# Performance work log

Hardware: AMD Instinct MI355X
Metric: run time of the kernel (lower is better)

## Reference

```python
import jax, jax.numpy as jnp
import numpy as np

V, E, H, D, A = 10000, 256, 256, 256, 256  # vocab, emb, enc_hid, dec_hid, attn_dim
B, S = 128, 64


def setup_inputs() -> dict:
    key = jax.random.key(0)
    ks = jax.random.split(key, 20)
    rn = lambda k, shp, sc: jax.random.normal(k, shp, jnp.float32) * sc
    tokens = jax.random.randint(ks[0], (B, S), 0, V, dtype=jnp.int32)
    inp = jnp.stack([tokens, jnp.ones_like(tokens)], axis=-1)  # [B,S,2], ch1 = mask
    s = 0.05
    return {
        "input": inp,
        "emb_table": rn(ks[1], (V, E), s),
        "enc_Wih_f": rn(ks[2], (3 * H, E), s), "enc_Whh_f": rn(ks[3], (3 * H, H), s),
        "enc_bih_f": rn(ks[4], (3 * H,), s), "enc_bhh_f": rn(ks[5], (3 * H,), s),
        "enc_Wih_b": rn(ks[6], (3 * H, E), s), "enc_Whh_b": rn(ks[7], (3 * H, H), s),
        "enc_bih_b": rn(ks[8], (3 * H,), s), "enc_bhh_b": rn(ks[9], (3 * H,), s),
        "enc_fc_W": rn(ks[10], (D, 2 * H), s), "enc_fc_b": rn(ks[11], (D,), s),
        "attn_W": rn(ks[12], (A, 2 * H + D), s), "attn_b": rn(ks[13], (A,), s),
        "dec_Wih": rn(ks[14], (3 * D, 2 * H + E), s), "dec_Whh": rn(ks[15], (3 * D, D), s),
        "dec_bih": rn(ks[16], (3 * D,), s), "dec_bhh": rn(ks[17], (3 * D,), s),
        "out_W": rn(ks[18], (V, 2 * H + D + E), s), "out_b": rn(ks[19], (V,), s),
    }


def _gru_cell(xp, h, Whh, bhh):
    # xp = x @ Wih.T + bih already computed; PyTorch gate order r,z,n
    rx, zx, nx = jnp.split(xp, 3, axis=-1)
    rh, zh, nh = jnp.split(h @ Whh.T + bhh, 3, axis=-1)
    r = jax.nn.sigmoid(rx + rh)
    z = jax.nn.sigmoid(zx + zh)
    n = jnp.tanh(nx + r * nh)
    return (1.0 - z) * n + z * h


def _gru_dir(x, Wih, Whh, bih, bhh, reverse):
    # x: [B,S,E] -> outputs [B,S,Hd], final hidden [B,Hd]
    xp = jnp.einsum('bse,ge->bsg', x, Wih) + bih  # [B,S,3Hd]
    Hd = Whh.shape[1]

    def step(h, xpt):
        h = _gru_cell(xpt, h, Whh, bhh)
        return h, h

    h0 = jnp.zeros((x.shape[0], Hd), x.dtype)
    hT, ys = jax.lax.scan(step, h0, jnp.swapaxes(xp, 0, 1), reverse=reverse)
    return jnp.swapaxes(ys, 0, 1), hT


def reference(input, emb_table, enc_Wih_f, enc_Whh_f, enc_bih_f, enc_bhh_f,
              enc_Wih_b, enc_Whh_b, enc_bih_b, enc_bhh_b, enc_fc_W, enc_fc_b,
              attn_W, attn_b, dec_Wih, dec_Whh, dec_bih, dec_bhh, out_W, out_b):
    b, s = input.shape[0], input.shape[1]
    v = emb_table.shape[0]
    tok = input[:, :, 0]
    mask = input[:, :, 1].astype(jnp.float32)
    emb = emb_table[tok] * mask[:, :, None]  # [B,S,E]

    # bidirectional encoder
    f_out, f_h = _gru_dir(emb, enc_Wih_f, enc_Whh_f, enc_bih_f, enc_bhh_f, False)
    b_out, b_h = _gru_dir(emb, enc_Wih_b, enc_Whh_b, enc_bih_b, enc_bhh_b, True)
    enc_out = jnp.concatenate([f_out, b_out], axis=-1)  # [B,S,2H]
    hidden = jnp.tanh(jnp.concatenate([f_h, b_h], axis=-1) @ enc_fc_W.T + enc_fc_b)  # [B,D]

    d = hidden.shape[1]

    def dec_step(carry, _):
        tok_t, h = carry
        e = emb_table[tok_t]  # [B,E]
        rep = jnp.concatenate(
            [jnp.broadcast_to(h[:, None, :], (b, s, d)), enc_out], axis=-1)
        energy = jnp.tanh(jnp.einsum('bsf,af->bsa', rep, attn_W) + attn_b)
        a = jax.nn.softmax(jnp.sum(energy, axis=-1), axis=1)  # [B,S]
        w = jnp.einsum('bs,bsh->bh', a, enc_out)  # [B,2H]
        rnn_in = jnp.concatenate([e, w], axis=-1)
        xp = rnn_in @ dec_Wih.T + dec_bih
        h_new = _gru_cell(xp, h, dec_Whh, dec_bhh)
        logits = jnp.concatenate([h_new, w, e], axis=-1) @ out_W.T + out_b  # [B,V]
        tok_new = jnp.argmax(logits, axis=-1).astype(tok_t.dtype)
        return (tok_new, h_new), logits

    tok0 = jnp.zeros((b,), jnp.int32)
    (_, _), outs = jax.lax.scan(dec_step, (tok0, hidden), None, length=s - 1)
    first = jnp.zeros((b, v), jnp.float32).at[:, 0].set(1.0)  # outputs[:,0] one-hot
    outputs = jnp.concatenate([first[:, None, :], jnp.swapaxes(outs, 0, 1)], axis=1)
    return jax.nn.log_softmax(outputs.reshape(-1, v), axis=-1)
```

## Files before the change

### kernel.cpp

```cpp
#include <hip/hip_runtime.h>
#include <math.h>


__device__ __forceinline__ float dot4(const float4 a, const float4 b) {
    return fmaf(a.x, b.x, fmaf(a.y, b.y, fmaf(a.z, b.z, a.w * b.w)));
}

__global__ void embed_kernel(const int* __restrict__ inp, const float* __restrict__ table,
                             float* __restrict__ emb) {
    int bs = blockIdx.x;
    int tok = inp[bs * 2];
    float msk = (float)inp[bs * 2 + 1];
    emb[bs * 256 + threadIdx.x] = table[tok * 256 + threadIdx.x] * msk;
}

__global__ __launch_bounds__(256) void enc_step_kernel(
    const float* __restrict__ emb,
    const float* __restrict__ Wih_f, const float* __restrict__ Whh_f,
    const float* __restrict__ bih_f, const float* __restrict__ bhh_f,
    const float* __restrict__ Wih_b, const float* __restrict__ Whh_b,
    const float* __restrict__ bih_b, const float* __restrict__ bhh_b,
    const float* __restrict__ hin_f, float* __restrict__ hout_f,
    const float* __restrict__ hin_b, float* __restrict__ hout_b,
    float* __restrict__ enc_out, int step)
{
    const int dir = blockIdx.y;
    const float* Wih = dir ? Wih_b : Wih_f;
    const float* Whh = dir ? Whh_b : Whh_f;
    const float* bih = dir ? bih_b : bih_f;
    const float* bhh = dir ? bhh_b : bhh_f;
    const float* hin = dir ? hin_b : hin_f;
    float* hout = dir ? hout_b : hout_f;
    const int t = dir ? (63 - step) : step;

    const int tid = threadIdx.x;
    const int dl = tid & 31;
    const int bsub = tid >> 5;
    const int d0 = (blockIdx.x & 7) * 32;
    const int b0 = (blockIdx.x >> 3) * 8;
    const int d = d0 + dl;
    const int b = b0 + bsub;

    __shared__ float xs[8][256];
    __shared__ float hs[8][256];
    for (int i = tid; i < 2048; i += 256) {
        int bl = i >> 8, e = i & 255;
        int bb = b0 + bl;
        xs[bl][e] = emb[(bb * 64 + t) * 256 + e];
        hs[bl][e] = hin[bb * 256 + e];
    }
    __syncthreads();

    const float4* x4 = (const float4*)xs[bsub];
    const float4* h4 = (const float4*)hs[bsub];
    const float4* wr_i = (const float4*)(Wih + (size_t)d * 256);
    const float4* wz_i = (const float4*)(Wih + (size_t)(256 + d) * 256);
    const float4* wn_i = (const float4*)(Wih + (size_t)(512 + d) * 256);
    const float4* wr_h = (const float4*)(Whh + (size_t)d * 256);
    const float4* wz_h = (const float4*)(Whh + (size_t)(256 + d) * 256);
    const float4* wn_h = (const float4*)(Whh + (size_t)(512 + d) * 256);

    float rs = 0.f, zs = 0.f, nx = 0.f, nh = 0.f;
    for (int k = 0; k < 64; ++k) {
        float4 xv = x4[k];
        float4 hv = h4[k];
        rs += dot4(xv, wr_i[k]) + dot4(hv, wr_h[k]);
        zs += dot4(xv, wz_i[k]) + dot4(hv, wz_h[k]);
        nx += dot4(xv, wn_i[k]);
        nh += dot4(hv, wn_h[k]);
    }
    rs += bih[d] + bhh[d];
    zs += bih[256 + d] + bhh[256 + d];
    nx += bih[512 + d];
    nh += bhh[512 + d];

    float r = 1.0f / (1.0f + expf(-rs));
    float z = 1.0f / (1.0f + expf(-zs));
    float n = tanhf(nx + r * nh);
    float hprev = hs[bsub][d];
    float hn = (1.0f - z) * n + z * hprev;

    hout[b * 256 + d] = hn;
    enc_out[(b * 64 + t) * 512 + dir * 256 + d] = hn;
}

__global__ __launch_bounds__(256) void enc_fc_kernel(
    const float* __restrict__ hf, const float* __restrict__ hb,
    const float* __restrict__ W, const float* __restrict__ bias,
    float* __restrict__ hdec0)
{
    int b = blockIdx.x, tid = threadIdx.x;
    __shared__ float xs[512];
    xs[tid] = hf[b * 256 + tid];
    xs[256 + tid] = hb[b * 256 + tid];
    __syncthreads();
    const float4* w4 = (const float4*)(W + (size_t)tid * 512);
    const float4* x4 = (const float4*)xs;
    float s = 0.f;
    for (int k = 0; k < 128; ++k) s += dot4(x4[k], w4[k]);
    hdec0[b * 256 + tid] = tanhf(s + bias[tid]);
}

#define GP 68
__global__ __launch_bounds__(256) void gemm2_kernel(
    const float* __restrict__ Amat, int lda,
    const float* __restrict__ Wmat, int ldw,
    const float* __restrict__ bias,
    float* __restrict__ C, long ldc,
    int N, int K)
{
    const int tid = threadIdx.x;
    const int tn = tid & 15;
    const int tm = tid >> 4;
    const long m0 = (long)blockIdx.y * 64;
    const int n0 = blockIdx.x * 64;
    __shared__ float As[64][GP];
    __shared__ float Ws[64][GP];

    const float* Abase = Amat + (m0 + tm) * lda + tn * 4;
    float4 ar[4], wr[4];
    float acc[4][4] = {};

    {
#pragma unroll
        for (int q = 0; q < 4; ++q)
            ar[q] = *(const float4*)(Abase + (long)16 * q * lda);
#pragma unroll
        for (int q = 0; q < 4; ++q) {
            int n = n0 + tm + 16 * q;
            wr[q] = (n < N) ? *(const float4*)(Wmat + (long)n * ldw + tn * 4)
                            : make_float4(0.f, 0.f, 0.f, 0.f);
        }
    }

    int k0 = 0;
    while (true) {
#pragma unroll
        for (int q = 0; q < 4; ++q) {
            *(float4*)&As[tm + 16 * q][tn * 4] = ar[q];
            *(float4*)&Ws[tm + 16 * q][tn * 4] = wr[q];
        }
        __syncthreads();

        const int kn = k0 + 64;
        if (kn < K) {
#pragma unroll
            for (int q = 0; q < 4; ++q)
                ar[q] = *(const float4*)(Abase + (long)16 * q * lda + kn);
#pragma unroll
            for (int q = 0; q < 4; ++q) {
                int n = n0 + tm + 16 * q;
                wr[q] = (n < N) ? *(const float4*)(Wmat + (long)n * ldw + tn * 4 + kn)
                                : make_float4(0.f, 0.f, 0.f, 0.f);
            }
        }

#pragma unroll
        for (int kk = 0; kk < 64; kk += 4) {
            float4 av[4], wv[4];
#pragma unroll
            for (int i = 0; i < 4; ++i) av[i] = *(const float4*)&As[tm + 16 * i][kk];
#pragma unroll
            for (int j = 0; j < 4; ++j) wv[j] = *(const float4*)&Ws[tn + 16 * j][kk];
#pragma unroll
            for (int i = 0; i < 4; ++i)
#pragma unroll
                for (int j = 0; j < 4; ++j)
                    acc[i][j] += dot4(av[i], wv[j]);
        }

        if (kn >= K) break;
        __syncthreads();
        k0 = kn;
    }

#pragma unroll
    for (int i = 0; i < 4; ++i) {
        long m = m0 + tm + 16 * i;
#pragma unroll
        for (int j = 0; j < 4; ++j) {
            int n = n0 + tn + 16 * j;
            if (n < N) C[m * ldc + n] = acc[i][j] + bias[n];
        }
    }
}

__global__ __launch_bounds__(256) void attn_kernel(
    const float* __restrict__ hprev, const float* __restrict__ attn_W,
    const float* __restrict__ enc_att, const float* __restrict__ enc_out,
    float* __restrict__ feat)
{
    const int b = blockIdx.x, tid = threadIdx.x;
    __shared__ float hsh[256];
    __shared__ float hE[256];
    __shared__ float part[256];
    __shared__ float aw[64];

    hsh[tid] = hprev[b * 256 + tid];
    __syncthreads();
    {
        const float4* w4 = (const float4*)(attn_W + (size_t)tid * 768);
        const float4* h4 = (const float4*)hsh;
        float s = 0.f;
        for (int k = 0; k < 64; ++k) s += dot4(h4[k], w4[k]);
        hE[tid] = s;
    }
    __syncthreads();
    {
        const int si = tid & 63, g = tid >> 6;
        const float* ea = enc_att + ((size_t)b * 64 + si) * 256 + g * 64;
        const float* he = hE + g * 64;
        float p = 0.f;
        for (int a = 0; a < 64; ++a) p += tanhf(he[a] + ea[a]);
        part[tid] = p;
    }
    __syncthreads();
    if (tid < 64) {
        float sc = part[tid] + part[64 + tid] + part[128 + tid] + part[192 + tid];
        float m = sc;
        for (int off = 32; off; off >>= 1) m = fmaxf(m, __shfl_xor(m, off));
        float ex = expf(sc - m);
        float sum = ex;
        for (int off = 32; off; off >>= 1) sum += __shfl_xor(sum, off);
        aw[tid] = ex / sum;
    }
    __syncthreads();
    {
        float w0 = 0.f, w1 = 0.f;
        for (int s2 = 0; s2 < 64; ++s2) {
            float as = aw[s2];
            const float* eo = enc_out + ((size_t)b * 64 + s2) * 512;
            w0 = fmaf(as, eo[tid], w0);
            w1 = fmaf(as, eo[256 + tid], w1);
        }
        feat[b * 1024 + 256 + tid] = w0;
        feat[b * 1024 + 512 + tid] = w1;
    }
}

__global__ __launch_bounds__(256) void dec_gru_kernel(
    const float* __restrict__ feat, const float* __restrict__ hin,
    const float* __restrict__ Wih, const float* __restrict__ Whh,
    const float* __restrict__ bih, const float* __restrict__ bhh,
    float* __restrict__ hout, float* __restrict__ feat_h)
{
    const int tid = threadIdx.x;
    const int dl = tid & 31, bsub = tid >> 5;
    const int d0 = (blockIdx.x & 7) * 32, b0 = (blockIdx.x >> 3) * 8;
    const int d = d0 + dl, b = b0 + bsub;

    __shared__ float rin[8][768];
    __shared__ float hsh[8][256];
    for (int i = tid; i < 2048; i += 256) {
        int bl = i >> 8, k = i & 255;
        rin[bl][k] = feat[(b0 + bl) * 1024 + 768 + k];
    }
    for (int i = tid; i < 4096; i += 256) {
        int bl = i >> 9, k = i & 511;
        rin[bl][256 + k] = feat[(b0 + bl) * 1024 + 256 + k];
    }
    for (int i = tid; i < 2048; i += 256) {
        int bl = i >> 8, k = i & 255;
        hsh[bl][k] = hin[(b0 + bl) * 256 + k];
    }
    __syncthreads();

    const float4* xv4 = (const float4*)rin[bsub];
    const float4* hv4 = (const float4*)hsh[bsub];
    const float4* Wr = (const float4*)(Wih + (size_t)d * 768);
    const float4* Wz = (const float4*)(Wih + (size_t)(256 + d) * 768);
    const float4* Wn = (const float4*)(Wih + (size_t)(512 + d) * 768);
    const float4* Ur = (const float4*)(Whh + (size_t)d * 256);
    const float4* Uz = (const float4*)(Whh + (size_t)(256 + d) * 256);
    const float4* Un = (const float4*)(Whh + (size_t)(512 + d) * 256);

    float rs = 0.f, zs = 0.f, nx = 0.f, nh = 0.f;
    for (int k = 0; k < 192; ++k) {
        float4 xv = xv4[k];
        rs += dot4(xv, Wr[k]);
        zs += dot4(xv, Wz[k]);
        nx += dot4(xv, Wn[k]);
    }
    for (int k = 0; k < 64; ++k) {
        float4 hv = hv4[k];
        rs += dot4(hv, Ur[k]);
        zs += dot4(hv, Uz[k]);
        nh += dot4(hv, Un[k]);
    }
    rs += bih[d] + bhh[d];
    zs += bih[256 + d] + bhh[256 + d];
    nx += bih[512 + d];
    nh += bhh[512 + d];

    float r = 1.0f / (1.0f + expf(-rs));
    float z = 1.0f / (1.0f + expf(-zs));
    float n = tanhf(nx + r * nh);
    float hprev = hsh[bsub][d];
    float hn = (1.0f - z) * n + z * hprev;

    hout[b * 256 + d] = hn;
    feat_h[b * 1024 + d] = hn;
}

__global__ __launch_bounds__(256) void argmax_kernel(
    const float* __restrict__ logits, const float* __restrict__ table,
    int* __restrict__ tok, float* __restrict__ feat)
{
    const int b = blockIdx.x, tid = threadIdx.x;
    const float4* row4 = (const float4*)(logits + (long)b * 640000);
    float best = -3.402823466e38f;
    int bi = 0;
    for (int v4 = tid; v4 < 2500; v4 += 256) {
        float4 x = row4[v4];
        int base = v4 << 2;
        if (x.x > best) { best = x.x; bi = base; }
        if (x.y > best) { best = x.y; bi = base + 1; }
        if (x.z > best) { best = x.z; bi = base + 2; }
        if (x.w > best) { best = x.w; bi = base + 3; }
    }
    __shared__ float bv[256];
    __shared__ int bix[256];
    bv[tid] = best; bix[tid] = bi;
    __syncthreads();
    for (int s2 = 128; s2; s2 >>= 1) {
        if (tid < s2) {
            float o = bv[tid + s2]; int oi = bix[tid + s2];
            if (o > bv[tid] || (o == bv[tid] && oi < bix[tid])) { bv[tid] = o; bix[tid] = oi; }
        }
        __syncthreads();
    }
    int t0 = bix[0];
    if (tid == 0) tok[b] = t0;
    feat[b * 1024 + 768 + tid] = table[(size_t)t0 * 256 + tid];
}

__global__ void init_e_kernel(const float* __restrict__ table, float* __restrict__ feat) {
    feat[blockIdx.x * 1024 + 768 + threadIdx.x] = table[threadIdx.x];
}

__global__ __launch_bounds__(256) void logsoftmax_kernel(float* __restrict__ out) {
    const int row = blockIdx.x;
    float* p = out + (long)row * 10000;
    const int tid = threadIdx.x;
    __shared__ float red[256];

    if ((row & 63) == 0) {
        float lse = logf(expf(1.0f) + 9999.0f);
        for (int v = tid; v < 10000; v += 256) p[v] = (v == 0 ? 1.0f : 0.0f) - lse;
        return;
    }

    float vals[40];
    float m = -3.402823466e38f;
#pragma unroll
    for (int i = 0; i < 40; ++i) {
        int v = tid + (i << 8);
        vals[i] = (v < 10000) ? p[v] : -3.402823466e38f;
        m = fmaxf(m, vals[i]);
    }
    red[tid] = m; __syncthreads();
    for (int s2 = 128; s2; s2 >>= 1) { if (tid < s2) red[tid] = fmaxf(red[tid], red[tid + s2]); __syncthreads(); }
    m = red[0]; __syncthreads();

    float sum = 0.f;
#pragma unroll
    for (int i = 0; i < 40; ++i) {
        int v = tid + (i << 8);
        if (v < 10000) sum += expf(vals[i] - m);
    }
    red[tid] = sum; __syncthreads();
    for (int s2 = 128; s2; s2 >>= 1) { if (tid < s2) red[tid] += red[tid + s2]; __syncthreads(); }
    float lse = m + logf(red[0]);

#pragma unroll
    for (int i = 0; i < 40; ++i) {
        int v = tid + (i << 8);
        if (v < 10000) p[v] = vals[i] - lse;
    }
}

extern "C" void kernel_launch(void* const* d_in, const int* in_sizes, int n_in,
                              void* d_out, int out_size, void* d_ws, size_t ws_size,
                              hipStream_t stream)
{
    const int*   inp      = (const int*)d_in[0];
    const float* emb_tab  = (const float*)d_in[1];
    const float* eWih_f   = (const float*)d_in[2];
    const float* eWhh_f   = (const float*)d_in[3];
    const float* ebih_f   = (const float*)d_in[4];
    const float* ebhh_f   = (const float*)d_in[5];
    const float* eWih_b   = (const float*)d_in[6];
    const float* eWhh_b   = (const float*)d_in[7];
    const float* ebih_b   = (const float*)d_in[8];
    const float* ebhh_b   = (const float*)d_in[9];
    const float* fc_W     = (const float*)d_in[10];
    const float* fc_b     = (const float*)d_in[11];
    const float* attn_W   = (const float*)d_in[12];
    const float* attn_b   = (const float*)d_in[13];
    const float* dWih     = (const float*)d_in[14];
    const float* dWhh     = (const float*)d_in[15];
    const float* dbih     = (const float*)d_in[16];
    const float* dbhh     = (const float*)d_in[17];
    const float* out_W    = (const float*)d_in[18];
    const float* out_b    = (const float*)d_in[19];

    float* ws = (float*)d_ws;
    float* emb     = ws;
    float* enc_out = emb + 2097152;
    float* enc_att = enc_out + 4194304;
    float* hf      = enc_att + 2097152;
    float* hb      = hf + 65536;
    float* hdec    = hb + 65536;
    float* feat    = hdec + 65536;
    int*   tok     = (int*)(feat + 131072);
    float* out     = (float*)d_out;

    embed_kernel<<<8192, 256, 0, stream>>>(inp, emb_tab, emb);
    hipMemsetAsync(hf, 0, 32768 * sizeof(float), stream);
    hipMemsetAsync(hb, 0, 32768 * sizeof(float), stream);
    for (int i = 0; i < 64; ++i) {
        const float* hinf = hf + (i & 1) * 32768;
        float* houtf = hf + ((i + 1) & 1) * 32768;
        const float* hinb = hb + (i & 1) * 32768;
        float* houtb = hb + ((i + 1) & 1) * 32768;
        enc_step_kernel<<<dim3(128, 2), 256, 0, stream>>>(
            emb, eWih_f, eWhh_f, ebih_f, ebhh_f, eWih_b, eWhh_b, ebih_b, ebhh_b,
            hinf, houtf, hinb, houtb, enc_out, i);
    }
    enc_fc_kernel<<<128, 256, 0, stream>>>(hf, hb, fc_W, fc_b, hdec);

    gemm2_kernel<<<dim3(4, 128), 256, 0, stream>>>(
        enc_out, 512, attn_W + 256, 768, attn_b, enc_att, 256, 256, 512);

    init_e_kernel<<<128, 256, 0, stream>>>(emb_tab, feat);

    for (int t = 1; t < 64; ++t) {
        const float* hprev = hdec + ((t - 1) & 1) * 32768;
        float* hcur = hdec + (t & 1) * 32768;
        attn_kernel<<<128, 256, 0, stream>>>(hprev, attn_W, enc_att, enc_out, feat);
        dec_gru_kernel<<<128, 256, 0, stream>>>(feat, hprev, dWih, dWhh, dbih, dbhh, hcur, feat);
        gemm2_kernel<<<dim3(157, 2), 256, 0, stream>>>(
            feat, 1024, out_W, 1024, out_b, out + (long)t * 10000, 640000, 10000, 1024);
        if (t < 63)
            argmax_kernel<<<128, 256, 0, stream>>>(out + (long)t * 10000, emb_tab, tok, feat);
    }

    logsoftmax_kernel<<<8192, 256, 0, stream>>>(out);
}
```

Baseline: 20.00 ms.

## Replace per-step encoder and decoder launches with persistent cooperative grid-sync kernels

The 64 encoder step launches and the roughly 250 decoder launches (attention, GRU, output GEMM, argmax) are replaced by two persistent cooperative kernels that loop over time steps and use grid.sync between phases. In the decoder, argmax for step t and attention for step t+1 run on disjoint block ranges in the same phase, and the output GEMM tiles are spread over all resident blocks. The aim is to remove kernel launch overhead and idle gaps between the many small dependent kernels. In exchange each step pays for grid-wide barriers, and the cooperative launch can fail if the grid does not fit, in which case the code falls back to the old launch loops.

```diff
diff --git a/kernel.cpp b/kernel.cpp
--- a/kernel.cpp
+++ b/kernel.cpp
@@ -1,5 +1,8 @@
 #include <hip/hip_runtime.h>
+#include <hip/hip_cooperative_groups.h>
 #include <math.h>
+
+namespace cg = cooperative_groups;
 
 
 __device__ __forceinline__ float dot4(const float4 a, const float4 b) {
@@ -12,6 +15,65 @@
     int tok = inp[bs * 2];
     float msk = (float)inp[bs * 2 + 1];
     emb[bs * 256 + threadIdx.x] = table[tok * 256 + threadIdx.x] * msk;
+}
+
+__device__ __forceinline__ void enc_step_phase(
+    int dir, int bx, int step,
+    const float* __restrict__ emb,
+    const float* __restrict__ Wih, const float* __restrict__ Whh,
+    const float* __restrict__ bih, const float* __restrict__ bhh,
+    const float* __restrict__ hin, float* __restrict__ hout,
+    float* __restrict__ enc_out,
+    float (*xs)[256], float (*hs)[256])
+{
+    const int t = dir ? (63 - step) : step;
+    const int tid = threadIdx.x;
+    const int dl = tid & 31;
+    const int bsub = tid >> 5;
+    const int d0 = (bx & 7) * 32;
+    const int b0 = (bx >> 3) * 8;
+    const int d = d0 + dl;
+    const int b = b0 + bsub;
+
+    for (int i = tid; i < 2048; i += 256) {
+        int bl = i >> 8, e = i & 255;
+        int bb = b0 + bl;
+        xs[bl][e] = emb[(bb * 64 + t) * 256 + e];
+        hs[bl][e] = hin[bb * 256 + e];
+    }
+    __syncthreads();
+
+    const float4* x4 = (const float4*)xs[bsub];
+    const float4* h4 = (const float4*)hs[bsub];
+    const float4* wr_i = (const float4*)(Wih + (size_t)d * 256);
+    const float4* wz_i = (const float4*)(Wih + (size_t)(256 + d) * 256);
+    const float4* wn_i = (const float4*)(Wih + (size_t)(512 + d) * 256);
+    const float4* wr_h = (const float4*)(Whh + (size_t)d * 256);
+    const float4* wz_h = (const float4*)(Whh + (size_t)(256 + d) * 256);
+    const float4* wn_h = (const float4*)(Whh + (size_t)(512 + d) * 256);
+
+    float rs = 0.f, zs = 0.f, nx = 0.f, nh = 0.f;
+    for (int k = 0; k < 64; ++k) {
+        float4 xv = x4[k];
+        float4 hv = h4[k];
+        rs += dot4(xv, wr_i[k]) + dot4(hv, wr_h[k]);
+        zs += dot4(xv, wz_i[k]) + dot4(hv, wz_h[k]);
+        nx += dot4(xv, wn_i[k]);
+        nh += dot4(hv, wn_h[k]);
+    }
+    rs += bih[d] + bhh[d];
+    zs += bih[256 + d] + bhh[256 + d];
+    nx += bih[512 + d];
+    nh += bhh[512 + d];
+
+    float r = 1.0f / (1.0f + expf(-rs));
+    float z = 1.0f / (1.0f + expf(-zs));
+    float n = tanhf(nx + r * nh);
+    float hprev = hs[bsub][d];
+    float hn = (1.0f - z) * n + z * hprev;
+
+    hout[b * 256 + d] = hn;
+    enc_out[(b * 64 + t) * 512 + dir * 256 + d] = hn;
 }
 
 __global__ __launch_bounds__(256) void enc_step_kernel(
@@ -25,63 +87,42 @@
     float* __restrict__ enc_out, int step)
 {
     const int dir = blockIdx.y;
+    __shared__ __align__(16) float xs[8][256];
+    __shared__ __align__(16) float hs[8][256];
+    enc_step_phase(dir, blockIdx.x, step, emb,
+                   dir ? Wih_b : Wih_f, dir ? Whh_b : Whh_f,
+                   dir ? bih_b : bih_f, dir ? bhh_b : bhh_f,
+                   dir ? hin_b : hin_f, dir ? hout_b : hout_f,
+                   enc_out, xs, hs);
+}
+
+__global__ __launch_bounds__(256) void enc_loop_kernel(
+    const float* __restrict__ emb,
+    const float* __restrict__ Wih_f, const float* __restrict__ Whh_f,
+    const float* __restrict__ bih_f, const float* __restrict__ bhh_f,
+    const float* __restrict__ Wih_b, const float* __restrict__ Whh_b,
+    const float* __restrict__ bih_b, const float* __restrict__ bhh_b,
+    float* __restrict__ hf, float* __restrict__ hb,
+    float* __restrict__ enc_out)
+{
+    cg::grid_group grid = cg::this_grid();
+    const int dir = blockIdx.x & 1;
+    const int bx = blockIdx.x >> 1;
     const float* Wih = dir ? Wih_b : Wih_f;
     const float* Whh = dir ? Whh_b : Whh_f;
     const float* bih = dir ? bih_b : bih_f;
     const float* bhh = dir ? bhh_b : bhh_f;
-    const float* hin = dir ? hin_b : hin_f;
-    float* hout = dir ? hout_b : hout_f;
-    const int t = dir ? (63 - step) : step;
-
-    const int tid = threadIdx.x;
-    const int dl = tid & 31;
-    const int bsub = tid >> 5;
-    const int d0 = (blockIdx.x & 7) * 32;
-    const int b0 = (blockIdx.x >> 3) * 8;
-    const int d = d0 + dl;
-    const int b = b0 + bsub;
-
-    __shared__ float xs[8][256];
-    __shared__ float hs[8][256];
-    for (int i = tid; i < 2048; i += 256) {
-        int bl = i >> 8, e = i & 255;
-        int bb = b0 + bl;
-        xs[bl][e] = emb[(bb * 64 + t) * 256 + e];
-        hs[bl][e] = hin[bb * 256 + e];
-    }
-    __syncthreads();
-
-    const float4* x4 = (const float4*)xs[bsub];
-    const float4* h4 = (const float4*)hs[bsub];
-    const float4* wr_i = (const float4*)(Wih + (size_t)d * 256);
-    const float4* wz_i = (const float4*)(Wih + (size_t)(256 + d) * 256);
-    const float4* wn_i = (const float4*)(Wih + (size_t)(512 + d) * 256);
-    const float4* wr_h = (const float4*)(Whh + (size_t)d * 256);
-    const float4* wz_h = (const float4*)(Whh + (size_t)(256 + d) * 256);
-    const float4* wn_h = (const float4*)(Whh + (size_t)(512 + d) * 256);
-
-    float rs = 0.f, zs = 0.f, nx = 0.f, nh = 0.f;
-    for (int k = 0; k < 64; ++k) {
-        float4 xv = x4[k];
-        float4 hv = h4[k];
-        rs += dot4(xv, wr_i[k]) + dot4(hv, wr_h[k]);
-        zs += dot4(xv, wz_i[k]) + dot4(hv, wz_h[k]);
-        nx += dot4(xv, wn_i[k]);
-        nh += dot4(hv, wn_h[k]);
-    }
-    rs += bih[d] + bhh[d];
-    zs += bih[256 + d] + bhh[256 + d];
-    nx += bih[512 + d];
-    nh += bhh[512 + d];
-
-    float r = 1.0f / (1.0f + expf(-rs));
-    float z = 1.0f / (1.0f + expf(-zs));
-    float n = tanhf(nx + r * nh);
-    float hprev = hs[bsub][d];
-    float hn = (1.0f - z) * n + z * hprev;
-
-    hout[b * 256 + d] = hn;
-    enc_out[(b * 64 + t) * 512 + dir * 256 + d] = hn;
+    float* hbase = dir ? hb : hf;
+
+    __shared__ __align__(16) float xs[8][256];
+    __shared__ __align__(16) float hs[8][256];
+
+    for (int i = 0; i < 64; ++i) {
+        const float* hin = hbase + (i & 1) * 32768;
+        float* hout = hbase + ((i + 1) & 1) * 32768;
+        enc_step_phase(dir, bx, i, emb, Wih, Whh, bih, bhh, hin, hout, enc_out, xs, hs);
+        if (i != 63) grid.sync();
+    }
 }
 
 __global__ __launch_bounds__(256) void enc_fc_kernel(
@@ -90,7 +131,7 @@
     float* __restrict__ hdec0)
 {
     int b = blockIdx.x, tid = threadIdx.x;
-    __shared__ float xs[512];
+    __shared__ __align__(16) float xs[512];
     xs[tid] = hf[b * 256 + tid];
     xs[256 + tid] = hb[b * 256 + tid];
     __syncthreads();
@@ -102,6 +143,88 @@
 }
 
 #define GP 68
+__device__ __forceinline__ void gemm_tile(
+    const float* __restrict__ Amat, int lda,
+    const float* __restrict__ Wmat, int ldw,
+    const float* __restrict__ bias,
+    float* __restrict__ C, long ldc,
+    int N, int K, long m0, int n0,
+    float (*As)[GP], float (*Ws)[GP])
+{
+    const int tid = threadIdx.x;
+    const int tn = tid & 15;
+    const int tm = tid >> 4;
+
+    __syncthreads();
+
+    const float* Abase = Amat + (m0 + tm) * lda + tn * 4;
+    float4 ar[4], wr[4];
+    float acc[4][4] = {};
+
+    {
+#pragma unroll
+        for (int q = 0; q < 4; ++q)
+            ar[q] = *(const float4*)(Abase + (long)16 * q * lda);
+#pragma unroll
+        for (int q = 0; q < 4; ++q) {
+            int n = n0 + tm + 16 * q;
+            wr[q] = (n < N) ? *(const float4*)(Wmat + (long)n * ldw + tn * 4)
+                            : make_float4(0.f, 0.f, 0.f, 0.f);
+        }
+    }
+
+    int k0 = 0;
+    while (true) {
+#pragma unroll
+        for (int q = 0; q < 4; ++q) {
+            *(float4*)&As[tm + 16 * q][tn * 4] = ar[q];
+            *(float4*)&Ws[tm + 16 * q][tn * 4] = wr[q];
+        }
+        __syncthreads();
+
+        const int kn = k0 + 64;
+        if (kn < K) {
+#pragma unroll
+            for (int q = 0; q < 4; ++q)
+                ar[q] = *(const float4*)(Abase + (long)16 * q * lda + kn);
+#pragma unroll
+            for (int q = 0; q < 4; ++q) {
+                int n = n0 + tm + 16 * q;
+                wr[q] = (n < N) ? *(const float4*)(Wmat + (long)n * ldw + tn * 4 + kn)
+                                : make_float4(0.f, 0.f, 0.f, 0.f);
+            }
+        }
+
+#pragma unroll
+        for (int kk = 0; kk < 64; kk += 4) {
+            float4 av[4], wv[4];
+#pragma unroll
+            for (int i = 0; i < 4; ++i) av[i] = *(const float4*)&As[tm + 16 * i][kk];
+#pragma unroll
+            for (int j = 0; j < 4; ++j) wv[j] = *(const float4*)&Ws[tn + 16 * j][kk];
+#pragma unroll
+            for (int i = 0; i < 4; ++i)
+#pragma unroll
+                for (int j = 0; j < 4; ++j)
+                    acc[i][j] += dot4(av[i], wv[j]);
+        }
+
+        if (kn >= K) break;
+        __syncthreads();
+        k0 = kn;
+    }
+
+#pragma unroll
+    for (int i = 0; i < 4; ++i) {
+        long m = m0 + tm + 16 * i;
+#pragma unroll
+        for (int j = 0; j < 4; ++j) {
+            int n = n0 + tn + 16 * j;
+            if (n < N) C[m * ldc + n] = acc[i][j] + bias[n];
+        }
+    }
+}
+
 __global__ __launch_bounds__(256) void gemm2_kernel(
     const float* __restrict__ Amat, int lda,
     const float* __restrict__ Wmat, int ldw,
@@ -109,93 +232,20 @@
     float* __restrict__ C, long ldc,
     int N, int K)
 {
+    __shared__ __align__(16) float As[64][GP];
+    __shared__ __align__(16) float Ws[64][GP];
+    gemm_tile(Amat, lda, Wmat, ldw, bias, C, ldc, N, K,
+              (long)blockIdx.y * 64, blockIdx.x * 64, As, Ws);
+}
+
+__device__ __forceinline__ void attn_phase(
+    int b, const float* __restrict__ hprev, const float* __restrict__ attn_W,
+    const float* __restrict__ enc_att, const float* __restrict__ enc_out,
+    float* __restrict__ feat,
+    float* __restrict__ hsh, float* __restrict__ hE,
+    float* __restrict__ part, float* __restrict__ aw)
+{
     const int tid = threadIdx.x;
-    const int tn = tid & 15;
-    const int tm = tid >> 4;
-    const long m0 = (long)blockIdx.y * 64;
-    const int n0 = blockIdx.x * 64;
-    __shared__ float As[64][GP];
-    __shared__ float Ws[64][GP];
-
-    const float* Abase = Amat + (m0 + tm) * lda + tn * 4;
-    float4 ar[4], wr[4];
-    float acc[4][4] = {};
-
-    {
-#pragma unroll
-        for (int q = 0; q < 4; ++q)
-            ar[q] = *(const float4*)(Abase + (long)16 * q * lda);
-#pragma unroll
-        for (int q = 0; q < 4; ++q) {
-            int n = n0 + tm + 16 * q;
-            wr[q] = (n < N) ? *(const float4*)(Wmat + (long)n * ldw + tn * 4)
-                            : make_float4(0.f, 0.f, 0.f, 0.f);
-        }
-    }
-
-    int k0 = 0;
-    while (true) {
-#pragma unroll
-        for (int q = 0; q < 4; ++q) {
-            *(float4*)&As[tm + 16 * q][tn * 4] = ar[q];
-            *(float4*)&Ws[tm + 16 * q][tn * 4] = wr[q];
-        }
-        __syncthreads();
-
-        const int kn = k0 + 64;
-        if (kn < K) {
-#pragma unroll
-            for (int q = 0; q < 4; ++q)
-                ar[q] = *(const float4*)(Abase + (long)16 * q * lda + kn);
-#pragma unroll
-            for (int q = 0; q < 4; ++q) {
-                int n = n0 + tm + 16 * q;
-                wr[q] = (n < N) ? *(const float4*)(Wmat + (long)n * ldw + tn * 4 + kn)
-                                : make_float4(0.f, 0.f, 0.f, 0.f);
-            }
-        }
-
-#pragma unroll
-        for (int kk = 0; kk < 64; kk += 4) {
-            float4 av[4], wv[4];
-#pragma unroll
-            for (int i = 0; i < 4; ++i) av[i] = *(const float4*)&As[tm + 16 * i][kk];
-#pragma unroll
-            for (int j = 0; j < 4; ++j) wv[j] = *(const float4*)&Ws[tn + 16 * j][kk];
-#pragma unroll
-            for (int i = 0; i < 4; ++i)
-#pragma unroll
-                for (int j = 0; j < 4; ++j)
-                    acc[i][j] += dot4(av[i], wv[j]);
-        }
-
-        if (kn >= K) break;
-        __syncthreads();
-        k0 = kn;
-    }
-
-#pragma unroll
-    for (int i = 0; i < 4; ++i) {
-        long m = m0 + tm + 16 * i;
-#pragma unroll
-        for (int j = 0; j < 4; ++j) {
-            int n = n0 + tn + 16 * j;
-            if (n < N) C[m * ldc + n] = acc[i][j] + bias[n];
-        }
-    }
-}
-
-__global__ __launch_bounds__(256) void attn_kernel(
-    const float* __restrict__ hprev, const float* __restrict__ attn_W,
-    const float* __restrict__ enc_att, const float* __restrict__ enc_out,
-    float* __restrict__ feat)
-{
-    const int b = blockIdx.x, tid = threadIdx.x;
-    __shared__ float hsh[256];
-    __shared__ float hE[256];
-    __shared__ float part[256];
-    __shared__ float aw[64];
-
     hsh[tid] = hprev[b * 256 + tid];
     __syncthreads();
     {
@@ -238,19 +288,30 @@
     }
 }
 
-__global__ __launch_bounds__(256) void dec_gru_kernel(
-    const float* __restrict__ feat, const float* __restrict__ hin,
+__global__ __launch_bounds__(256) void attn_kernel(
+    const float* __restrict__ hprev, const float* __restrict__ attn_W,
+    const float* __restrict__ enc_att, const float* __restrict__ enc_out,
+    float* __restrict__ feat)
+{
+    __shared__ __align__(16) float hsh[256];
+    __shared__ __align__(16) float hE[256];
+    __shared__ __align__(16) float part[256];
+    __shared__ __align__(16) float aw[64];
+    attn_phase(blockIdx.x, hprev, attn_W, enc_att, enc_out, feat, hsh, hE, part, aw);
+}
+
+__device__ __forceinline__ void gru_phase(
+    int bx, const float* __restrict__ feat, const float* __restrict__ hin,
     const float* __restrict__ Wih, const float* __restrict__ Whh,
     const float* __restrict__ bih, const float* __restrict__ bhh,
-    float* __restrict__ hout, float* __restrict__ feat_h)
+    float* __restrict__ hout, float* __restrict__ feat_h,
+    float (*rin)[768], float (*hsh)[256])
 {
     const int tid = threadIdx.x;
     const int dl = tid & 31, bsub = tid >> 5;
-    const int d0 = (blockIdx.x & 7) * 32, b0 = (blockIdx.x >> 3) * 8;
+    const int d0 = (bx & 7) * 32, b0 = (bx >> 3) * 8;
     const int d = d0 + dl, b = b0 + bsub;
 
-    __shared__ float rin[8][768];
-    __shared__ float hsh[8][256];
     for (int i = tid; i < 2048; i += 256) {
         int bl = i >> 8, k = i & 255;
         rin[bl][k] = feat[(b0 + bl) * 1024 + 768 + k];
@@ -302,11 +363,23 @@
     feat_h[b * 1024 + d] = hn;
 }
 
-__global__ __launch_bounds__(256) void argmax_kernel(
-    const float* __restrict__ logits, const float* __restrict__ table,
-    int* __restrict__ tok, float* __restrict__ feat)
-{
-    const int b = blockIdx.x, tid = threadIdx.x;
+__global__ __launch_bounds__(256) void dec_gru_kernel(
+    const float* __restrict__ feat, const float* __restrict__ hin,
+    const float* __restrict__ Wih, const float* __restrict__ Whh,
+    const float* __restrict__ bih, const float* __restrict__ bhh,
+    float* __restrict__ hout, float* __restrict__ feat_h)
+{
+    __shared__ __align__(16) float rin[8][768];
+    __shared__ __align__(16) float hsh[8][256];
+    gru_phase(blockIdx.x, feat, hin, Wih, Whh, bih, bhh, hout, feat_h, rin, hsh);
+}
+
+__device__ __forceinline__ void argmax_phase(
+    int b, const float* __restrict__ logits, const float* __restrict__ table,
+    int* __restrict__ tok, float* __restrict__ feat,
+    float* __restrict__ bv, int* __restrict__ bix)
+{
+    const int tid = threadIdx.x;
     const float4* row4 = (const float4*)(logits + (long)b * 640000);
     float best = -3.402823466e38f;
     int bi = 0;
@@ -318,8 +391,6 @@
         if (x.z > best) { best = x.z; bi = base + 2; }
         if (x.w > best) { best = x.w; bi = base + 3; }
     }
-    __shared__ float bv[256];
-    __shared__ int bix[256];
     bv[tid] = best; bix[tid] = bi;
     __syncthreads();
     for (int s2 = 128; s2; s2 >>= 1) {
@@ -334,8 +405,73 @@
     feat[b * 1024 + 768 + tid] = table[(size_t)t0 * 256 + tid];
 }
 
+__global__ __launch_bounds__(256) void argmax_kernel(
+    const float* __restrict__ logits, const float* __restrict__ table,
+    int* __restrict__ tok, float* __restrict__ feat)
+{
+    __shared__ __align__(16) float bv[256];
+    __shared__ __align__(16) int bix[256];
+    argmax_phase(blockIdx.x, logits, table, tok, feat, bv, bix);
+}
+
 __global__ void init_e_kernel(const float* __restrict__ table, float* __restrict__ feat) {
     feat[blockIdx.x * 1024 + 768 + threadIdx.x] = table[threadIdx.x];
+}
+
+__global__ __launch_bounds__(256, 2) void dec_loop_kernel(
+    const float* __restrict__ emb_tab, const float* __restrict__ attn_W,
+    const float* __restrict__ dWih, const float* __restrict__ dWhh,
+    const float* __restrict__ dbih, const float* __restrict__ dbhh,
+    const float* __restrict__ out_W, const float* __restrict__ out_b,
+    const float* __restrict__ enc_out, const float* __restrict__ enc_att,
+    float* __restrict__ hdec, float* __restrict__ feat,
+    int* __restrict__ tok, float* __restrict__ out)
+{
+    cg::grid_group grid = cg::this_grid();
+    const int bid = blockIdx.x;
+    const int nb = gridDim.x;
+    const int tid = threadIdx.x;
+
+    __shared__ __align__(16) union SMem {
+        struct { float hsh[256]; float hE[256]; float part[256]; float aw[64]; } at;
+        struct { float rin[8][768]; float hsh[8][256]; } gr;
+        struct { float As[64][GP]; float Ws[64][GP]; } gm;
+        struct { float bv[256]; int bix[256]; } am;
+    } sm;
+
+    if (bid < 128) {
+        feat[bid * 1024 + 768 + tid] = emb_tab[tid];
+        attn_phase(bid, hdec, attn_W, enc_att, enc_out, feat,
+                   sm.at.hsh, sm.at.hE, sm.at.part, sm.at.aw);
+    }
+    grid.sync();
+
+    for (int t = 1; t < 64; ++t) {
+        const float* hprev = hdec + ((t - 1) & 1) * 32768;
+        float* hcur = hdec + (t & 1) * 32768;
+
+        if (bid < 128)
+            gru_phase(bid, feat, hprev, dWih, dWhh, dbih, dbhh, hcur, feat,
+                      sm.gr.rin, sm.gr.hsh);
+        grid.sync();
+
+        float* Crow = out + (long)t * 10000;
+        for (int tile = bid; tile < 314; tile += nb) {
+            gemm_tile(feat, 1024, out_W, 1024, out_b, Crow, 640000,
+                      10000, 1024, (long)(tile & 1) * 64, (tile >> 1) * 64,
+                      sm.gm.As, sm.gm.Ws);
+        }
+
+        if (t < 63) {
+            grid.sync();
+            if (bid < 128)
+                argmax_phase(bid, Crow, emb_tab, tok, feat, sm.am.bv, sm.am.bix);
+            else if (bid < 256)
+                attn_phase(bid - 128, hcur, attn_W, enc_att, enc_out, feat,
+                           sm.at.hsh, sm.at.hE, sm.at.part, sm.at.aw);
+            grid.sync();
+        }
+    }
 }
 
 __global__ __launch_bounds__(256) void logsoftmax_kernel(float* __restrict__ out) {
@@ -418,31 +554,55 @@
     embed_kernel<<<8192, 256, 0, stream>>>(inp, emb_tab, emb);
     hipMemsetAsync(hf, 0, 32768 * sizeof(float), stream);
     hipMemsetAsync(hb, 0, 32768 * sizeof(float), stream);
-    for (int i = 0; i < 64; ++i) {
-        const float* hinf = hf + (i & 1) * 32768;
-        float* houtf = hf + ((i + 1) & 1) * 32768;
-        const float* hinb = hb + (i & 1) * 32768;
-        float* houtb = hb + ((i + 1) & 1) * 32768;
-        enc_step_kernel<<<dim3(128, 2), 256, 0, stream>>>(
-            emb, eWih_f, eWhh_f, ebih_f, ebhh_f, eWih_b, eWhh_b, ebih_b, ebhh_b,
-            hinf, houtf, hinb, houtb, enc_out, i);
+
+    {
+        void* ea[] = {
+            (void*)&emb, (void*)&eWih_f, (void*)&eWhh_f, (void*)&ebih_f, (void*)&ebhh_f,
+            (void*)&eWih_b, (void*)&eWhh_b, (void*)&ebih_b, (void*)&ebhh_b,
+            (void*)&hf, (void*)&hb, (void*)&enc_out };
+        hipError_t err = hipLaunchCooperativeKernel(enc_loop_kernel, dim3(256), dim3(256),
+                                                    ea, 0, stream);
+        if (err != hipSuccess) {
+            for (int i = 0; i < 64; ++i) {
+                const float* hinf = hf + (i & 1) * 32768;
+                float* houtf = hf + ((i + 1) & 1) * 32768;
+                const float* hinb = hb + (i & 1) * 32768;
+                float* houtb = hb + ((i + 1) & 1) * 32768;
+                enc_step_kernel<<<dim3(128, 2), 256, 0, stream>>>(
+                    emb, eWih_f, eWhh_f, ebih_f, ebhh_f, eWih_b, eWhh_b, ebih_b, ebhh_b,
+                    hinf, houtf, hinb, houtb, enc_out, i);
+            }
+        }
     }
     enc_fc_kernel<<<128, 256, 0, stream>>>(hf, hb, fc_W, fc_b, hdec);
 
     gemm2_kernel<<<dim3(4, 128), 256, 0, stream>>>(
         enc_out, 512, attn_W + 256, 768, attn_b, enc_att, 256, 256, 512);
 
-    init_e_kernel<<<128, 256, 0, stream>>>(emb_tab, feat);
-
-    for (int t = 1; t < 64; ++t) {
-        const float* hprev = hdec + ((t - 1) & 1) * 32768;
-        float* hcur = hdec + (t & 1) * 32768;
-        attn_kernel<<<128, 256, 0, stream>>>(hprev, attn_W, enc_att, enc_out, feat);
-        dec_gru_kernel<<<128, 256, 0, stream>>>(feat, hprev, dWih, dWhh, dbih, dbhh, hcur, feat);
-        gemm2_kernel<<<dim3(157, 2), 256, 0, stream>>>(
-            feat, 1024, out_W, 1024, out_b, out + (long)t * 10000, 640000, 10000, 1024);
-        if (t < 63)
-            argmax_kernel<<<128, 256, 0, stream>>>(out + (long)t * 10000, emb_tab, tok, feat);
+    {
+        void* da[] = {
+            (void*)&emb_tab, (void*)&attn_W, (void*)&dWih, (void*)&dWhh,
+            (void*)&dbih, (void*)&dbhh, (void*)&out_W, (void*)&out_b,
+            (void*)&enc_out, (void*)&enc_att, (void*)&hdec, (void*)&feat,
+            (void*)&tok, (void*)&out };
+        hipError_t err = hipLaunchCooperativeKernel(dec_loop_kernel, dim3(512), dim3(256),
+                                                    da, 0, stream);
+        if (err != hipSuccess)
+            err = hipLaunchCooperativeKernel(dec_loop_kernel, dim3(256), dim3(256),
+                                             da, 0, stream);
+        if (err != hipSuccess) {
+            init_e_kernel<<<128, 256, 0, stream>>>(emb_tab, feat);
+            for (int t = 1; t < 64; ++t) {
+                const float* hprev = hdec + ((t - 1) & 1) * 32768;
+                float* hcur = hdec + (t & 1) * 32768;
+                attn_kernel<<<128, 256, 0, stream>>>(hprev, attn_W, enc_att, enc_out, feat);
+                dec_gru_kernel<<<128, 256, 0, stream>>>(feat, hprev, dWih, dWhh, dbih, dbhh, hcur, feat);
+                gemm2_kernel<<<dim3(157, 2), 256, 0, stream>>>(
+                    feat, 1024, out_W, 1024, out_b, out + (long)t * 10000, 640000, 10000, 1024);
+                if (t < 63)
+                    argmax_kernel<<<128, 256, 0, stream>>>(out + (long)t * 10000, emb_tab, tok, feat);
+            }
+        }
     }
 
     logsoftmax_kernel<<<8192, 256, 0, stream>>>(out);
```

Result: slower. 47.95 ms (+139.7%).

## Merge argmax with next-step attention and retile output projection to 80 columns

Applied to the files above, without the earlier changes.

Attention for the next decoder step depends only on the new hidden state, so it now runs in the same launch as the argmax/embedding lookup. A single 256-block kernel does both, which removes one launch per step and lets the two phases share the GPU. The output projection uses a new fixed-shape GEMM with 64x80 tiles, so 10000 columns split into exactly 125 tiles with no bounds checks. The wider tiles raise per-thread register and shared-memory use.

```diff
diff --git a/kernel.cpp b/kernel.cpp
--- a/kernel.cpp
+++ b/kernel.cpp
@@ -41,8 +41,8 @@
     const int d = d0 + dl;
     const int b = b0 + bsub;
 
-    __shared__ float xs[8][256];
-    __shared__ float hs[8][256];
+    __shared__ __align__(16) float xs[8][256];
+    __shared__ __align__(16) float hs[8][256];
     for (int i = tid; i < 2048; i += 256) {
         int bl = i >> 8, e = i & 255;
         int bb = b0 + bl;
@@ -90,7 +90,7 @@
     float* __restrict__ hdec0)
 {
     int b = blockIdx.x, tid = threadIdx.x;
-    __shared__ float xs[512];
+    __shared__ __align__(16) float xs[512];
     xs[tid] = hf[b * 256 + tid];
     xs[256 + tid] = hb[b * 256 + tid];
     __syncthreads();
@@ -114,8 +114,8 @@
     const int tm = tid >> 4;
     const long m0 = (long)blockIdx.y * 64;
     const int n0 = blockIdx.x * 64;
-    __shared__ float As[64][GP];
-    __shared__ float Ws[64][GP];
+    __shared__ __align__(16) float As[64][GP];
+    __shared__ __align__(16) float Ws[64][GP];
 
     const float* Abase = Amat + (m0 + tm) * lda + tn * 4;
     float4 ar[4], wr[4];
@@ -185,17 +185,90 @@
     }
 }
 
-__global__ __launch_bounds__(256) void attn_kernel(
-    const float* __restrict__ hprev, const float* __restrict__ attn_W,
+__global__ __launch_bounds__(256) void gemm80_kernel(
+    const float* __restrict__ Amat, const float* __restrict__ Wmat,
+    const float* __restrict__ bias, float* __restrict__ C)
+{
+    const int tid = threadIdx.x;
+    const int tn = tid & 15;
+    const int tm = tid >> 4;
+    const long m0 = (long)blockIdx.y * 64;
+    const int n0 = blockIdx.x * 80;
+    __shared__ __align__(16) float As[64][GP];
+    __shared__ __align__(16) float Ws[80][GP];
+
+    const float* Abase = Amat + (m0 + tm) * 1024 + tn * 4;
+    const float* Wbase = Wmat + (long)(n0 + tm) * 1024 + tn * 4;
+    float4 ar[4], wr[5];
+    float acc[4][5] = {};
+
+    {
+#pragma unroll
+        for (int q = 0; q < 4; ++q)
+            ar[q] = *(const float4*)(Abase + (long)16 * q * 1024);
+#pragma unroll
+        for (int q = 0; q < 5; ++q)
+            wr[q] = *(const float4*)(Wbase + (long)16 * q * 1024);
+    }
+
+    int k0 = 0;
+    while (true) {
+#pragma unroll
+        for (int q = 0; q < 4; ++q)
+            *(float4*)&As[tm + 16 * q][tn * 4] = ar[q];
+#pragma unroll
+        for (int q = 0; q < 5; ++q)
+            *(float4*)&Ws[tm + 16 * q][tn * 4] = wr[q];
+        __syncthreads();
+
+        const int kn = k0 + 64;
+        if (kn < 1024) {
+#pragma unroll
+            for (int q = 0; q < 4; ++q)
+                ar[q] = *(const float4*)(Abase + (long)16 * q * 1024 + kn);
+#pragma unroll
+            for (int q = 0; q < 5; ++q)
+                wr[q] = *(const float4*)(Wbase + (long)16 * q * 1024 + kn);
+        }
+
+#pragma unroll
+        for (int kk = 0; kk < 64; kk += 4) {
+            float4 av[4], wv[5];
+#pragma unroll
+            for (int i = 0; i < 4; ++i) av[i] = *(const float4*)&As[tm + 16 * i][kk];
+#pragma unroll
+            for (int j = 0; j < 5; ++j) wv[j] = *(const float4*)&Ws[tn + 16 * j][kk];
+#pragma unroll
+            for (int i = 0; i < 4; ++i)
+#pragma unroll
+                for (int j = 0; j < 5; ++j)
+                    acc[i][j] += dot4(av[i], wv[j]);
+        }
+
+        if (kn >= 1024) break;
+        __syncthreads();
+        k0 = kn;
+    }
+
+#pragma unroll
+    for (int i = 0; i < 4; ++i) {
+        long m = m0 + tm + 16 * i;
+#pragma unroll
+        for (int j = 0; j < 5; ++j) {
+            int n = n0 + tn + 16 * j;
+            C[m * 640000 + n] = acc[i][j] + bias[n];
+        }
+    }
+}
+
+__device__ __forceinline__ void attn_phase(
+    int b, const float* __restrict__ hprev, const float* __restrict__ attn_W,
     const float* __restrict__ enc_att, const float* __restrict__ enc_out,
-    float* __restrict__ feat)
-{
-    const int b = blockIdx.x, tid = threadIdx.x;
-    __shared__ float hsh[256];
-    __shared__ float hE[256];
-    __shared__ float part[256];
-    __shared__ float aw[64];
-
+    float* __restrict__ feat,
+    float* __restrict__ hsh, float* __restrict__ hE,
+    float* __restrict__ part, float* __restrict__ aw)
+{
+    const int tid = threadIdx.x;
     hsh[tid] = hprev[b * 256 + tid];
     __syncthreads();
     {
@@ -238,75 +311,24 @@
     }
 }
 
-__global__ __launch_bounds__(256) void dec_gru_kernel(
-    const float* __restrict__ feat, const float* __restrict__ hin,
-    const float* __restrict__ Wih, const float* __restrict__ Whh,
-    const float* __restrict__ bih, const float* __restrict__ bhh,
-    float* __restrict__ hout, float* __restrict__ feat_h)
-{
-    const int tid = threadIdx.x;
-    const int dl = tid & 31, bsub = tid >> 5;
-    const int d0 = (blockIdx.x & 7) * 32, b0 = (blockIdx.x >> 3) * 8;
-    const int d = d0 + dl, b = b0 + bsub;
-
-    __shared__ float rin[8][768];
-    __shared__ float hsh[8][256];
-    for (int i = tid; i < 2048; i += 256) {
-        int bl = i >> 8, k = i & 255;
-        rin[bl][k] = feat[(b0 + bl) * 1024 + 768 + k];
-    }
-    for (int i = tid; i < 4096; i += 256) {
-        int bl = i >> 9, k = i & 511;
-        rin[bl][256 + k] = feat[(b0 + bl) * 1024 + 256 + k];
-    }
-    for (int i = tid; i < 2048; i += 256) {
-        int bl = i >> 8, k = i & 255;
-        hsh[bl][k] = hin[(b0 + bl) * 256 + k];
-    }
-    __syncthreads();
-
-    const float4* xv4 = (const float4*)rin[bsub];
-    const float4* hv4 = (const float4*)hsh[bsub];
-    const float4* Wr = (const float4*)(Wih + (size_t)d * 768);
-    const float4* Wz = (const float4*)(Wih + (size_t)(256 + d) * 768);
-    const float4* Wn = (const float4*)(Wih + (size_t)(512 + d) * 768);
-    const float4* Ur = (const float4*)(Whh + (size_t)d * 256);
-    const float4* Uz = (const float4*)(Whh + (size_t)(256 + d) * 256);
-    const float4* Un = (const float4*)(Whh + (size_t)(512 + d) * 256);
-
-    float rs = 0.f, zs = 0.f, nx = 0.f, nh = 0.f;
-    for (int k = 0; k < 192; ++k) {
-        float4 xv = xv4[k];
-        rs += dot4(xv, Wr[k]);
-        zs += dot4(xv, Wz[k]);
-        nx += dot4(xv, Wn[k]);
-    }
-    for (int k = 0; k < 64; ++k) {
-        float4 hv = hv4[k];
-        rs += dot4(hv, Ur[k]);
-        zs += dot4(hv, Uz[k]);
-        nh += dot4(hv, Un[k]);
-    }
-    rs += bih[d] + bhh[d];
-    zs += bih[256 + d] + bhh[256 + d];
-    nx += bih[512 + d];
-    nh += bhh[512 + d];
-
-    float r = 1.0f / (1.0f + expf(-rs));
-    float z = 1.0f / (1.0f + expf(-zs));
-    float n = tanhf(nx + r * nh);
-    float hprev = hsh[bsub][d];
-    float hn = (1.0f - z) * n + z * hprev;
-
-    hout[b * 256 + d] = hn;
-    feat_h[b * 1024 + d] = hn;
-}
-
-__global__ __launch_bounds__(256) void argmax_kernel(
-    const float* __restrict__ logits, const float* __restrict__ table,
-    int* __restrict__ tok, float* __restrict__ feat)
-{
-    const int b = blockIdx.x, tid = threadIdx.x;
+__global__ __launch_bounds__(256) void attn_kernel(
+    const float* __restrict__ hprev, const float* __restrict__ attn_W,
+    const float* __restrict__ enc_att, const float* __restrict__ enc_out,
+    float* __restrict__ feat)
+{
+    __shared__ __align__(16) float hsh[256];
+    __shared__ __align__(16) float hE[256];
+    __shared__ __align__(16) float part[256];
+    __shared__ __align__(16) float aw[64];
+    attn_phase(blockIdx.x, hprev, attn_W, enc_att, enc_out, feat, hsh, hE, part, aw);
+}
+
+__device__ __forceinline__ void argmax_phase(
+    int b, const float* __restrict__ logits, const float* __restrict__ table,
+    int* __restrict__ tok, float* __restrict__ feat,
+    float* __restrict__ bv, int* __restrict__ bix)
+{
+    const int tid = threadIdx.x;
     const float4* row4 = (const float4*)(logits + (long)b * 640000);
     float best = -3.402823466e38f;
     int bi = 0;
@@ -318,8 +340,6 @@
         if (x.z > best) { best = x.z; bi = base + 2; }
         if (x.w > best) { best = x.w; bi = base + 3; }
     }
-    __shared__ float bv[256];
-    __shared__ int bix[256];
     bv[tid] = best; bix[tid] = bi;
     __syncthreads();
     for (int s2 = 128; s2; s2 >>= 1) {
@@ -332,6 +352,88 @@
     int t0 = bix[0];
     if (tid == 0) tok[b] = t0;
     feat[b * 1024 + 768 + tid] = table[(size_t)t0 * 256 + tid];
+}
+
+__global__ __launch_bounds__(256) void post_kernel(
+    const float* __restrict__ logits, const float* __restrict__ table,
+    int* __restrict__ tok, float* __restrict__ feat,
+    const float* __restrict__ hcur, const float* __restrict__ attn_W,
+    const float* __restrict__ enc_att, const float* __restrict__ enc_out)
+{
+    __shared__ __align__(16) float s0[256];
+    __shared__ __align__(16) float s1[256];
+    __shared__ __align__(16) float s2[256];
+    __shared__ __align__(16) float s3[64];
+    __shared__ __align__(16) int   si[256];
+    const int bid = blockIdx.x;
+    if (bid < 128)
+        argmax_phase(bid, logits, table, tok, feat, s0, si);
+    else
+        attn_phase(bid - 128, hcur, attn_W, enc_att, enc_out, feat, s0, s1, s2, s3);
+}
+
+__global__ __launch_bounds__(256) void dec_gru_kernel(
+    const float* __restrict__ feat, const float* __restrict__ hin,
+    const float* __restrict__ Wih, const float* __restrict__ Whh,
+    const float* __restrict__ bih, const float* __restrict__ bhh,
+    float* __restrict__ hout, float* __restrict__ feat_h)
+{
+    const int tid = threadIdx.x;
+    const int dl = tid & 31, bsub = tid >> 5;
+    const int d0 = (blockIdx.x & 7) * 32, b0 = (blockIdx.x >> 3) * 8;
+    const int d = d0 + dl, b = b0 + bsub;
+
+    __shared__ __align__(16) float rin[8][768];
+    __shared__ __align__(16) float hsh[8][256];
+    for (int i = tid; i < 2048; i += 256) {
+        int bl = i >> 8, k = i & 255;
+        rin[bl][k] = feat[(b0 + bl) * 1024 + 768 + k];
+    }
+    for (int i = tid; i < 4096; i += 256) {
+        int bl = i >> 9, k = i & 511;
+        rin[bl][256 + k] = feat[(b0 + bl) * 1024 + 256 + k];
+    }
+    for (int i = tid; i < 2048; i += 256) {
+        int bl = i >> 8, k = i & 255;
+        hsh[bl][k] = hin[(b0 + bl) * 256 + k];
+    }
+    __syncthreads();
+
+    const float4* xv4 = (const float4*)rin[bsub];
+    const float4* hv4 = (const float4*)hsh[bsub];
+    const float4* Wr = (const float4*)(Wih + (size_t)d * 768);
+    const float4* Wz = (const float4*)(Wih + (size_t)(256 + d) * 768);
+    const float4* Wn = (const float4*)(Wih + (size_t)(512 + d) * 768);
+    const float4* Ur = (const float4*)(Whh + (size_t)d * 256);
+    const float4* Uz = (const float4*)(Whh + (size_t)(256 + d) * 256);
+    const float4* Un = (const float4*)(Whh + (size_t)(512 + d) * 256);
+
+    float rs = 0.f, zs = 0.f, nx = 0.f, nh = 0.f;
+    for (int k = 0; k < 192; ++k) {
+        float4 xv = xv4[k];
+        rs += dot4(xv, Wr[k]);
+        zs += dot4(xv, Wz[k]);
+        nx += dot4(xv, Wn[k]);
+    }
+    for (int k = 0; k < 64; ++k) {
+        float4 hv = hv4[k];
+        rs += dot4(hv, Ur[k]);
+        zs += dot4(hv, Uz[k]);
+        nh += dot4(hv, Un[k]);
+    }
+    rs += bih[d] + bhh[d];
+    zs += bih[256 + d] + bhh[256 + d];
+    nx += bih[512 + d];
+    nh += bhh[512 + d];
+
+    float r = 1.0f / (1.0f + expf(-rs));
+    float z = 1.0f / (1.0f + expf(-zs));
+    float n = tanhf(nx + r * nh);
+    float hprev = hsh[bsub][d];
+    float hn = (1.0f - z) * n + z * hprev;
+
+    hout[b * 256 + d] = hn;
+    feat_h[b * 1024 + d] = hn;
 }
 
 __global__ void init_e_kernel(const float* __restrict__ table, float* __restrict__ feat) {
@@ -433,16 +535,18 @@
         enc_out, 512, attn_W + 256, 768, attn_b, enc_att, 256, 256, 512);
 
     init_e_kernel<<<128, 256, 0, stream>>>(emb_tab, feat);
+    attn_kernel<<<128, 256, 0, stream>>>(hdec, attn_W, enc_att, enc_out, feat);
 
     for (int t = 1; t < 64; ++t) {
         const float* hprev = hdec + ((t - 1) & 1) * 32768;
         float* hcur = hdec + (t & 1) * 32768;
-        attn_kernel<<<128, 256, 0, stream>>>(hprev, attn_W, enc_att, enc_out, feat);
         dec_gru_kernel<<<128, 256, 0, stream>>>(feat, hprev, dWih, dWhh, dbih, dbhh, hcur, feat);
-        gemm2_kernel<<<dim3(157, 2), 256, 0, stream>>>(
-            feat, 1024, out_W, 1024, out_b, out + (long)t * 10000, 640000, 10000, 1024);
+        gemm80_kernel<<<dim3(125, 2), 256, 0, stream>>>(
+            feat, out_W, out_b, out + (long)t * 10000);
         if (t < 63)
-            argmax_kernel<<<128, 256, 0, stream>>>(out + (long)t * 10000, emb_tab, tok, feat);
+            post_kernel<<<256, 256, 0, stream>>>(
+                out + (long)t * 10000, emb_tab, tok, feat,
+                hcur, attn_W, enc_att, enc_out);
     }
 
     logsoftmax_kernel<<<8192, 256, 0, stream>>>(out);
```

New measurement: 17.46 ms. 12.7% less time.
